# Kernel optimization log

Measured on AMD Instinct MI355X. Metric: run time of the kernel, lower is better.

## Reference

```python
import jax, jax.numpy as jnp
import numpy as np

E = 768
H = 8
EXP = 4
HEAD_D = E // H  # 96, also the post-softmax scaling factor


def _layernorm(x, g, b, eps=1e-5):
    mu = jnp.mean(x, axis=-1, keepdims=True)
    var = jnp.var(x, axis=-1, keepdims=True)
    return (x - mu) * jax.lax.rsqrt(var + eps) * g + b


def setup_inputs() -> dict:
    key = jax.random.key(0)
    ks = jax.random.split(key, 12)
    s = 0.02
    inp = {
        "x": jax.random.normal(ks[0], (8, 1024, E), dtype=jnp.float32),
        "ln1_g": jnp.ones((E,), jnp.float32),
        "ln1_b": jnp.zeros((E,), jnp.float32),
        "Wq": jax.random.normal(ks[1], (E, E), jnp.float32) * s,
        "bq": jnp.zeros((E,), jnp.float32),
        "Wk": jax.random.normal(ks[2], (E, E), jnp.float32) * s,
        "bk": jnp.zeros((E,), jnp.float32),
        "Wv": jax.random.normal(ks[3], (E, E), jnp.float32) * s,
        "bv": jnp.zeros((E,), jnp.float32),
        "Wo": jax.random.normal(ks[4], (E, E), jnp.float32) * s,
        "bo": jnp.zeros((E,), jnp.float32),
        "ln2_g": jnp.ones((E,), jnp.float32),
        "ln2_b": jnp.zeros((E,), jnp.float32),
        "W1": jax.random.normal(ks[5], (E, EXP * E), jnp.float32) * s,
        "b1": jnp.zeros((EXP * E,), jnp.float32),
        "W2": jax.random.normal(ks[6], (EXP * E, E), jnp.float32) * s,
        "b2": jnp.zeros((E,), jnp.float32),
    }
    return inp


def reference(x, ln1_g, ln1_b, Wq, bq, Wk, bk, Wv, bv, Wo, bo,
              ln2_g, ln2_b, W1, b1, W2, b2):
    B, N, _ = x.shape
    # --- sub_block_1: LN -> MHA (post-softmax scaling) -> residual ---
    h = _layernorm(x, ln1_g, ln1_b)
    q = (h @ Wq + bq).reshape(B, N, H, HEAD_D).transpose(0, 2, 1, 3)
    k = (h @ Wk + bk).reshape(B, N, H, HEAD_D).transpose(0, 2, 1, 3)
    v = (h @ Wv + bv).reshape(B, N, H, HEAD_D).transpose(0, 2, 1, 3)
    energy = jnp.einsum('bhqd,bhkd->bhqk', q, k)  # NOTE: no pre-softmax scale
    att = jax.nn.softmax(energy, axis=-1) * HEAD_D  # quirky post-softmax scaling
    out = jnp.einsum('bhqk,bhkd->bhqd', att, v)
    out = out.transpose(0, 2, 1, 3).reshape(B, N, E)
    out = out @ Wo + bo
    x = x + out  # residual
    # --- sub_block_2: LN -> GELU-FFN (NO residual, faithful to source) ---
    h = _layernorm(x, ln2_g, ln2_b)
    h = jax.nn.gelu(h @ W1 + b1, approximate=False)
    return h @ W2 + b2
```

## Files before the change

### kernel.cpp

```cpp
#include <hip/hip_runtime.h>
#include <hip/hip_bf16.h>
#include <math.h>

#define DI __device__ __forceinline__

typedef __attribute__((ext_vector_type(8))) __bf16 bf16x8;
typedef __attribute__((ext_vector_type(8))) short short8;
typedef __attribute__((ext_vector_type(4))) float f32x4;
typedef __attribute__((ext_vector_type(4))) int int4v;
typedef __attribute__((ext_vector_type(4))) unsigned short ushort4v;

DI short f2bfn(float f) {
  __bf16 b = (__bf16)f;
  short s;
  __builtin_memcpy(&s, &b, 2);
  return s;
}

DI float erf_fast(float x) {
  const float ax = fabsf(x);
  const float t = __builtin_amdgcn_rcpf(1.0f + 0.3275911f * ax);
  float p = 1.061405429f;
  p = p * t - 1.453152027f;
  p = p * t + 1.421413741f;
  p = p * t - 0.284496736f;
  p = p * t + 0.254829592f;
  p = p * t;
  const float r = 1.0f - p * __expf(-ax * ax);
  return copysignf(r, x);
}

DI void gload_lds16(const void* g, void* l) {
  __builtin_amdgcn_global_load_lds(
      (const __attribute__((address_space(1))) void*)g,
      (__attribute__((address_space(3))) void*)l, 16, 0, 0);
}

__global__ __launch_bounds__(256) void weight_prep(
    const float* __restrict__ Wq, const float* __restrict__ Wk,
    const float* __restrict__ Wv, const float* __restrict__ Wo,
    const float* __restrict__ W1, const float* __restrict__ W2,
    const float* __restrict__ bq, const float* __restrict__ bk,
    const float* __restrict__ bv,
    short* __restrict__ Wtqkv, short* __restrict__ Wto,
    short* __restrict__ Wt1, short* __restrict__ Wt2,
    float* __restrict__ bqkv)
{
  const int id = blockIdx.x, t = threadIdx.x;
  if (id >= 6912) {
    const int j = id - 6912;
    const float* src = j == 0 ? bq : (j == 1 ? bk : bv);
    for (int e = t; e < 768; e += 256) bqkv[j * 768 + e] = src[e];
    return;
  }
  const float* in;
  short* out;
  int K, N, bx, by;
  if (id < 2304) {
    const int w = id / 576, r2 = id % 576;
    bx = r2 % 24; by = r2 / 24; K = 768; N = 768;
    in = (w == 0) ? Wq : (w == 1) ? Wk : (w == 2) ? Wv : Wo;
    out = (w < 3) ? Wtqkv + (size_t)w * 768 * 768 : Wto;
  } else if (id < 4608) {
    const int r2 = id - 2304;
    bx = r2 % 96; by = r2 / 96; K = 768; N = 3072; in = W1; out = Wt1;
  } else {
    const int r2 = id - 4608;
    bx = r2 % 24; by = r2 / 24; K = 3072; N = 768; in = W2; out = Wt2;
  }
  __shared__ float tile[32][33];
  const int tx = t & 31, ty = t >> 5;
  const int n0 = bx * 32, k0 = by * 32;
#pragma unroll
  for (int p = 0; p < 4; ++p)
    tile[ty + p * 8][tx] = in[(size_t)(k0 + ty + p * 8) * N + n0 + tx];
  __syncthreads();
#pragma unroll
  for (int p = 0; p < 4; ++p)
    out[(size_t)(n0 + ty + p * 8) * K + k0 + tx] = f2bfn(tile[tx][ty + p * 8]);
}

__global__ __launch_bounds__(256) void ln_rows(
    const float* __restrict__ x, const float* __restrict__ gw,
    const float* __restrict__ bw, unsigned short* __restrict__ out)
{
  const int wv = threadIdx.x >> 6, ln = threadIdx.x & 63;
  const size_t row = (size_t)blockIdx.x * 4 + wv;
  const float* xr = x + row * 768;
  float4 v[3];
  float s = 0.f, sq = 0.f;
#pragma unroll
  for (int i = 0; i < 3; ++i) {
    v[i] = *(const float4*)(xr + i * 256 + ln * 4);
    s  += v[i].x + v[i].y + v[i].z + v[i].w;
    sq += v[i].x * v[i].x + v[i].y * v[i].y + v[i].z * v[i].z + v[i].w * v[i].w;
  }
#pragma unroll
  for (int msk = 1; msk < 64; msk <<= 1) {
    s  += __shfl_xor(s, msk);
    sq += __shfl_xor(sq, msk);
  }
  const float mean = s * (1.f / 768.f);
  const float var  = sq * (1.f / 768.f) - mean * mean;
  const float rstd = rsqrtf(var + 1e-5f);
#pragma unroll
  for (int i = 0; i < 3; ++i) {
    const int c = i * 256 + ln * 4;
    const float vals[4] = {v[i].x, v[i].y, v[i].z, v[i].w};
    ushort4v o;
#pragma unroll
    for (int j = 0; j < 4; ++j)
      o[j] = (unsigned short)f2bfn((vals[j] - mean) * rstd * gw[c + j] + bw[c + j]);
    *(ushort4v*)(out + row * 768 + c) = o;
  }
}

enum { EPI_BF16 = 0, EPI_F32_RES = 1, EPI_BF16_GELU = 2, EPI_F32 = 3, EPI_QKV = 4 };

template <int MODE, int BM, int BK, int MW>
__global__ __launch_bounds__(256, MW) void gemm_bt(
    const short* __restrict__ A,
    const short* __restrict__ Bt,
    const float* __restrict__ bias,
    const float* __restrict__ resid,
    void* __restrict__ Cout, short* __restrict__ vTout,
    int ldc, int Ntiles, int K)
{
  constexpr int NCHUNK = BK / 8;
  constexpr int CMASK = NCHUNK - 1;
  constexpr int ABYTES = BM * BK * 2;
  constexpr int STAGE_BYTES = (BM + 128) * BK * 2;
  constexpr int NLA = BM * BK / 8 / 256;
  constexpr int NLB = 128 * BK / 8 / 256;
  constexpr int LOADS = NLA + NLB;
  constexpr int MR = BM / 32;
  constexpr int NKK = BK / 32;
  constexpr int SMEM = 2 * STAGE_BYTES > 4 * 4352 ? 2 * STAGE_BYTES : 4 * 4352;
  __shared__ __align__(16) char smem[SMEM];
  const int t = threadIdx.x;
  const int wv = t >> 6, ln = t & 63;
  const int g = ln >> 4, r = ln & 15;
  const int sw = ((int)blockIdx.x & 7) * ((int)gridDim.x >> 3) + ((int)blockIdx.x >> 3);
  const int bm = sw / Ntiles, bn = sw % Ntiles;
  const int wr = wv >> 1, wc = wv & 1;
  f32x4 acc[MR][4] = {};

  const char* aptr[NLA];
  const char* bptr[NLB];
#pragma unroll
  for (int q = 0; q < NLA; ++q) {
    const int p = q * 256 + t;
    const int row = p / NCHUNK, c = (p & CMASK) ^ (row & CMASK);
    aptr[q] = (const char*)(A + (size_t)(bm * BM + row) * K + c * 8);
  }
#pragma unroll
  for (int q = 0; q < NLB; ++q) {
    const int p = q * 256 + t;
    const int row = p / NCHUNK, c = (p & CMASK) ^ (row & CMASK);
    bptr[q] = (const char*)(Bt + (size_t)(bn * 128 + row) * K + c * 8);
  }

  auto stage = [&](int buf) {
    char* as = smem + buf * STAGE_BYTES;
    char* bs = as + ABYTES;
#pragma unroll
    for (int q = 0; q < NLA; ++q) {
      gload_lds16(aptr[q], as + q * 4096 + wv * 1024);
      aptr[q] += BK * 2;
    }
#pragma unroll
    for (int q = 0; q < NLB; ++q) {
      gload_lds16(bptr[q], bs + q * 4096 + wv * 1024);
      bptr[q] += BK * 2;
    }
  };

  const int nk = K / BK;
  stage(0);
  stage(1);
  int cur = 0;
  for (int kt = 0; kt < nk; ++kt) {
    if (kt + 1 < nk)
      asm volatile("s_waitcnt vmcnt(%0)\n\ts_barrier" :: "n"(LOADS) : "memory");
    else
      asm volatile("s_waitcnt vmcnt(0)\n\ts_barrier" ::: "memory");
    const short* as = (const short*)(smem + cur * STAGE_BYTES);
    const short* bs = as + ABYTES / 2;
    bf16x8 af[MR][NKK], bfr[4][NKK];
#pragma unroll
    for (int m = 0; m < MR; ++m) {
      const int row = wr * (BM / 2) + m * 16 + r;
#pragma unroll
      for (int kk = 0; kk < NKK; ++kk)
        af[m][kk] = *(const bf16x8*)(as + row * BK + (((kk * 4 + g) ^ (row & CMASK)) << 3));
    }
#pragma unroll
    for (int n = 0; n < 4; ++n) {
      const int row = wc * 64 + n * 16 + r;
#pragma unroll
      for (int kk = 0; kk < NKK; ++kk)
        bfr[n][kk] = *(const bf16x8*)(bs + row * BK + (((kk * 4 + g) ^ (row & CMASK)) << 3));
    }
#pragma unroll
    for (int kk = 0; kk < NKK; ++kk)
#pragma unroll
      for (int m = 0; m < MR; ++m)
#pragma unroll
        for (int n = 0; n < 4; ++n)
          acc[m][n] = __builtin_amdgcn_mfma_f32_16x16x32_bf16(af[m][kk], bfr[n][kk],
                                                              acc[m][n], 0, 0, 0);
    if (kt + 2 < nk) {
      asm volatile("s_waitcnt lgkmcnt(0)\n\ts_barrier" ::: "memory");
      stage(cur);
    }
    cur ^= 1;
  }
  __syncthreads();

  float* epi = (float*)(smem + wv * 4352);

  if constexpr (MODE == EPI_QKV) {
    if (bn * 128 >= 1536) {
      const int tc = ln;
      const int cglob = bn * 128 + wc * 64 + tc;
      const int cv = cglob - 1536;
      const float bvs = bias[cglob];
#pragma unroll
      for (int m = 0; m < MR; ++m) {
#pragma unroll
        for (int n = 0; n < 4; ++n)
#pragma unroll
          for (int q = 0; q < 4; ++q)
            epi[(g * 4 + q) * 68 + n * 16 + r] = acc[m][n][q];
        float tv[16];
#pragma unroll
        for (int row = 0; row < 16; ++row) tv[row] = epi[row * 68 + tc] + bvs;
        const int tokbase = bm * BM + wr * (BM / 2) + m * 16;
        const int bb = tokbase >> 10, toff = tokbase & 1023;
        short8 o0, o1;
#pragma unroll
        for (int e = 0; e < 8; ++e) { o0[e] = f2bfn(tv[e]); o1[e] = f2bfn(tv[e + 8]); }
        short* dst = vTout + ((size_t)(bb * 768 + cv)) * 1024 + toff;
        *(short8*)dst = o0;
        *(short8*)(dst + 8) = o1;
      }
      return;
    }
  }

  const int cq = (ln & 3) * 16;
  const int lr = ln >> 2;
  const int c0 = bn * 128 + wc * 64 + cq;
  f32x4 bv[4];
#pragma unroll
  for (int j = 0; j < 4; ++j) bv[j] = *(const f32x4*)(bias + c0 + j * 4);

#pragma unroll
  for (int m = 0; m < MR; ++m) {
#pragma unroll
    for (int n = 0; n < 4; ++n)
#pragma unroll
      for (int q = 0; q < 4; ++q)
        epi[(g * 4 + q) * 68 + n * 16 + r] = acc[m][n][q];
    const size_t grow = (size_t)(bm * BM + wr * (BM / 2) + m * 16 + lr);
    float vals[16];
#pragma unroll
    for (int j = 0; j < 4; ++j) {
      const f32x4 vv = *(const f32x4*)(epi + lr * 68 + cq + j * 4);
#pragma unroll
      for (int e = 0; e < 4; ++e) vals[j * 4 + e] = vv[e] + bv[j][e];
    }
    if constexpr (MODE == EPI_F32_RES) {
#pragma unroll
      for (int j = 0; j < 4; ++j) {
        const f32x4 rv = *(const f32x4*)(resid + grow * ldc + c0 + j * 4);
#pragma unroll
        for (int e = 0; e < 4; ++e) vals[j * 4 + e] += rv[e];
      }
    }
    if constexpr (MODE == EPI_BF16_GELU) {
#pragma unroll
      for (int j = 0; j < 16; ++j)
        vals[j] = 0.5f * vals[j] * (1.0f + erf_fast(vals[j] * 0.70710678118654752f));
    }
    if constexpr (MODE == EPI_F32 || MODE == EPI_F32_RES) {
      float* op = (float*)Cout + grow * ldc + c0;
#pragma unroll
      for (int j = 0; j < 4; ++j) {
        f32x4 ov;
#pragma unroll
        for (int e = 0; e < 4; ++e) ov[e] = vals[j * 4 + e];
        *(f32x4*)(op + j * 4) = ov;
      }
    } else {
      unsigned short* op = (unsigned short*)Cout + grow * ldc + c0;
#pragma unroll
      for (int hhalf = 0; hhalf < 2; ++hhalf) {
        short8 ov;
#pragma unroll
        for (int e = 0; e < 8; ++e) ov[e] = f2bfn(vals[hhalf * 8 + e]);
        *(short8*)(op + hhalf * 8) = ov;
      }
    }
  }
}

__global__ __launch_bounds__(256, 2) void attn_fwd(
    const short* __restrict__ qkv, const short* __restrict__ vT,
    unsigned short* __restrict__ ab)
{
  __shared__ short Ks[2][64 * 128];
  __shared__ short Vs[2][96 * 64];
  __shared__ short Ps[4][2][16 * 64];
  const int t = threadIdx.x, wv = t >> 6, ln = t & 63;
  const int g = ln >> 4, r = ln & 15;
  const int bid = ((int)blockIdx.x & 7) * 64 + ((int)blockIdx.x >> 3);
  const int bh = bid >> 3, qt = bid & 7;
  const int b = bh >> 3, h = bh & 7;

  bf16x8 qf[2][3];
#pragma unroll
  for (int u = 0; u < 2; ++u) {
    const size_t rowq = (size_t)(b * 1024 + qt * 128 + wv * 32 + u * 16 + r);
#pragma unroll
    for (int kd = 0; kd < 3; ++kd)
      qf[u][kd] = *(const bf16x8*)(qkv + rowq * 2304 + h * 96 + kd * 32 + g * 8);
  }

  size_t offK[4];
#pragma unroll
  for (int i = 0; i < 4; ++i) {
    const int p = i * 256 + t;
    const int row = p >> 4, cb = p & 15, cbs = cb ^ (row & 7);
    offK[i] = (size_t)row * 2304 + 768 + h * 96 + (cbs << 3);
  }
  size_t offV[3];
#pragma unroll
  for (int i = 0; i < 3; ++i) {
    const int p = i * 256 + t;
    const int row = p >> 3, cb = p & 7, cbs = cb ^ (row & 7);
    offV[i] = ((size_t)bh * 96 + row) * 1024 + (cbs << 3);
  }
  const short* qb = qkv + (size_t)b * 1024 * 2304;

  auto stageKV = [&](int buf, int kt) {
    const size_t kadd = (size_t)kt * 64 * 2304;
#pragma unroll
    for (int i = 0; i < 4; ++i)
      gload_lds16(qb + kadd + offK[i], (char*)Ks[buf] + i * 4096 + wv * 1024);
#pragma unroll
    for (int i = 0; i < 3; ++i)
      gload_lds16(vT + offV[i] + kt * 64, (char*)Vs[buf] + i * 4096 + wv * 1024);
  };

  f32x4 o[2][6] = {};
  float mr[2] = {-1e30f, -1e30f}, lr[2] = {0.f, 0.f};

  stageKV(0, 0);
  __syncthreads();
  int cur = 0;
  for (int kt = 0; kt < 16; ++kt) {
    if (kt < 15) stageKV(cur ^ 1, kt + 1);
    const short* ks = Ks[cur];
    const short* vs = Vs[cur];

    f32x4 s[2][4] = {};
    __builtin_amdgcn_s_setprio(1);
#pragma unroll
    for (int sub = 0; sub < 4; ++sub) {
      bf16x8 kf[3];
#pragma unroll
      for (int kd = 0; kd < 3; ++kd)
        kf[kd] = *(const bf16x8*)(
            ks + (sub * 16 + r) * 128 + (((kd * 4 + g) ^ (r & 7)) << 3));
#pragma unroll
      for (int u = 0; u < 2; ++u)
#pragma unroll
        for (int kd = 0; kd < 3; ++kd)
          s[u][sub] = __builtin_amdgcn_mfma_f32_16x16x32_bf16(kf[kd], qf[u][kd],
                                                              s[u][sub], 0, 0, 0);
    }
    __builtin_amdgcn_s_setprio(0);

#pragma unroll
    for (int u = 0; u < 2; ++u) {
      float tm = fmaxf(fmaxf(s[u][0][0], s[u][0][1]),
                       fmaxf(s[u][0][2], s[u][0][3]));
#pragma unroll
      for (int sub = 1; sub < 4; ++sub)
        tm = fmaxf(tm, fmaxf(fmaxf(s[u][sub][0], s[u][sub][1]),
                             fmaxf(s[u][sub][2], s[u][sub][3])));
      tm = fmaxf(tm, __shfl_xor(tm, 16));
      tm = fmaxf(tm, __shfl_xor(tm, 32));

      if (__any(tm > mr[u] + 8.f)) {
        const float mnew = fmaxf(mr[u], tm);
        const float sc = __expf(mr[u] - mnew);
        lr[u] *= sc;
        mr[u] = mnew;
        float scr[4];
#pragma unroll
        for (int reg = 0; reg < 4; ++reg)
          scr[reg] = __shfl(sc, (ln & 48) | (g * 4 + reg));
#pragma unroll
        for (int nd = 0; nd < 6; ++nd)
#pragma unroll
          for (int reg = 0; reg < 4; ++reg) o[u][nd][reg] *= scr[reg];
      }

      float tsum = 0.f;
#pragma unroll
      for (int sub = 0; sub < 4; ++sub) {
        float p0 = __expf(s[u][sub][0] - mr[u]);
        float p1 = __expf(s[u][sub][1] - mr[u]);
        float p2 = __expf(s[u][sub][2] - mr[u]);
        float p3 = __expf(s[u][sub][3] - mr[u]);
        tsum += (p0 + p1) + (p2 + p3);
        ushort4v pk;
        pk[0] = (unsigned short)f2bfn(p0);
        pk[1] = (unsigned short)f2bfn(p1);
        pk[2] = (unsigned short)f2bfn(p2);
        pk[3] = (unsigned short)f2bfn(p3);
        const int c8 = (sub * 4 + g) ^ ((r & 7) << 1);
        *(ushort4v*)((char*)Ps[wv][u] + r * 128 + c8 * 8) = pk;
      }
      tsum += __shfl_xor(tsum, 16);
      tsum += __shfl_xor(tsum, 32);
      lr[u] += tsum;
    }

    bf16x8 pf[2][2];
#pragma unroll
    for (int u = 0; u < 2; ++u)
#pragma unroll
      for (int kk = 0; kk < 2; ++kk)
        pf[u][kk] = *(const bf16x8*)(
            Ps[wv][u] + r * 64 + (((kk * 4 + g) ^ (r & 7)) << 3));
    __builtin_amdgcn_s_setprio(1);
#pragma unroll
    for (int nd = 0; nd < 6; ++nd) {
      bf16x8 vf[2];
#pragma unroll
      for (int kk = 0; kk < 2; ++kk)
        vf[kk] = *(const bf16x8*)(
            vs + (nd * 16 + r) * 64 + (((kk * 4 + g) ^ (r & 7)) << 3));
#pragma unroll
      for (int u = 0; u < 2; ++u)
#pragma unroll
        for (int kk = 0; kk < 2; ++kk)
          o[u][nd] = __builtin_amdgcn_mfma_f32_16x16x32_bf16(pf[u][kk], vf[kk],
                                                             o[u][nd], 0, 0, 0);
    }
    __builtin_amdgcn_s_setprio(0);

    __syncthreads();
    cur ^= 1;
  }

#pragma unroll
  for (int u = 0; u < 2; ++u) {
    float linv[4];
#pragma unroll
    for (int reg = 0; reg < 4; ++reg)
      linv[reg] = 96.0f / __shfl(lr[u], (ln & 48) | (g * 4 + reg));
#pragma unroll
    for (int reg = 0; reg < 4; ++reg) {
      const size_t row = (size_t)(b * 1024 + qt * 128 + wv * 32 + u * 16 + g * 4 + reg);
#pragma unroll
      for (int nd = 0; nd < 6; ++nd)
        ab[row * 768 + h * 96 + nd * 16 + r] =
            (unsigned short)f2bfn(o[u][nd][reg] * linv[reg]);
    }
  }
}

extern "C" void kernel_launch(void* const* d_in, const int* in_sizes, int n_in,
                              void* d_out, int out_size, void* d_ws, size_t ws_size,
                              hipStream_t stream)
{
  const float* x    = (const float*)d_in[0];
  const float* ln1g = (const float*)d_in[1];
  const float* ln1b = (const float*)d_in[2];
  const float* Wq   = (const float*)d_in[3];
  const float* bq   = (const float*)d_in[4];
  const float* Wk   = (const float*)d_in[5];
  const float* bk   = (const float*)d_in[6];
  const float* Wv   = (const float*)d_in[7];
  const float* bv   = (const float*)d_in[8];
  const float* Wo   = (const float*)d_in[9];
  const float* bo   = (const float*)d_in[10];
  const float* ln2g = (const float*)d_in[11];
  const float* ln2b = (const float*)d_in[12];
  const float* W1   = (const float*)d_in[13];
  const float* b1   = (const float*)d_in[14];
  const float* W2   = (const float*)d_in[15];
  const float* b2   = (const float*)d_in[16];

  char* ws = (char*)d_ws;
  size_t off = 0;
  short* Wtqkv = (short*)(ws + off); off += (size_t)2304 * 768 * 2;
  short* Wto   = (short*)(ws + off); off += (size_t)768 * 768 * 2;
  short* Wt1   = (short*)(ws + off); off += (size_t)3072 * 768 * 2;
  short* Wt2   = (short*)(ws + off); off += (size_t)768 * 3072 * 2;
  float* bqkv  = (float*)(ws + off); off += 16384;
  short* hb    = (short*)(ws + off); off += (size_t)8192 * 768 * 2;
  short* qkv   = (short*)(ws + off); off += (size_t)8192 * 2304 * 2;
  short* h2b   = (short*)(ws + off); off += (size_t)8192 * 768 * 2;
  short* f1 = hb;
  short* ab = hb;
  short* vT = h2b;
  float* x1 = (float*)d_out;

  weight_prep<<<6915, 256, 0, stream>>>(Wq, Wk, Wv, Wo, W1, W2, bq, bk, bv,
                                        Wtqkv, Wto, Wt1, Wt2, bqkv);

  ln_rows<<<2048, 256, 0, stream>>>(x, ln1g, ln1b, (unsigned short*)hb);
  gemm_bt<EPI_QKV, 128, 32, 4><<<64 * 18, 256, 0, stream>>>(
      hb, Wtqkv, bqkv, nullptr, qkv, vT, 2304, 18, 768);
  attn_fwd<<<512, 256, 0, stream>>>(qkv, vT, (unsigned short*)ab);
  gemm_bt<EPI_F32_RES, 64, 64, 3><<<128 * 6, 256, 0, stream>>>(
      ab, Wto, bo, x, x1, nullptr, 768, 6, 768);

  ln_rows<<<2048, 256, 0, stream>>>(x1, ln2g, ln2b, (unsigned short*)h2b);
  gemm_bt<EPI_BF16_GELU, 128, 32, 4><<<64 * 24, 256, 0, stream>>>(
      h2b, Wt1, b1, nullptr, f1, nullptr, 3072, 24, 768);
  gemm_bt<EPI_F32, 64, 64, 3><<<128 * 6, 256, 0, stream>>>(
      f1, Wt2, b2, nullptr, (float*)d_out, nullptr, 768, 6, 3072);
}
```

Measured before the change: 242.3 us.

## Triple-buffer LDS stages in BM=128 GEMMs to drop per-iteration barrier

Adds an NBUF template parameter to the GEMM kernel. The QKV and FFN1 GEMMs (BM=128, BK=32) now use three LDS stage buffers. With a third buffer, the next global-to-LDS prefetch can be issued before the MFMA loop, and the second lgkmcnt wait plus barrier per k-iteration can be dropped, so loads overlap compute better. In exchange LDS use per block grows to three stages, and the occupancy hint drops from 4 to 3 blocks per CU for those GEMMs.

```diff
diff --git a/kernel.cpp b/kernel.cpp
--- a/kernel.cpp
+++ b/kernel.cpp
@@ -117,7 +117,7 @@
 
 enum { EPI_BF16 = 0, EPI_F32_RES = 1, EPI_BF16_GELU = 2, EPI_F32 = 3, EPI_QKV = 4 };
 
-template <int MODE, int BM, int BK, int MW>
+template <int MODE, int BM, int BK, int MW, int NBUF>
 __global__ __launch_bounds__(256, MW) void gemm_bt(
     const short* __restrict__ A,
     const short* __restrict__ Bt,
@@ -135,7 +135,8 @@
   constexpr int LOADS = NLA + NLB;
   constexpr int MR = BM / 32;
   constexpr int NKK = BK / 32;
-  constexpr int SMEM = 2 * STAGE_BYTES > 4 * 4352 ? 2 * STAGE_BYTES : 4 * 4352;
+  constexpr int SMEM = NBUF * STAGE_BYTES > 4 * 4352 ? NBUF * STAGE_BYTES
+                                                     : 4 * 4352;
   __shared__ __align__(16) char smem[SMEM];
   const int t = threadIdx.x;
   const int wv = t >> 6, ln = t & 63;
@@ -178,13 +179,13 @@
   const int nk = K / BK;
   stage(0);
   stage(1);
-  int cur = 0;
+  int rb = 0;
   for (int kt = 0; kt < nk; ++kt) {
     if (kt + 1 < nk)
       asm volatile("s_waitcnt vmcnt(%0)\n\ts_barrier" :: "n"(LOADS) : "memory");
     else
       asm volatile("s_waitcnt vmcnt(0)\n\ts_barrier" ::: "memory");
-    const short* as = (const short*)(smem + cur * STAGE_BYTES);
+    const short* as = (const short*)(smem + rb * STAGE_BYTES);
     const short* bs = as + ABYTES / 2;
     bf16x8 af[MR][NKK], bfr[4][NKK];
 #pragma unroll
@@ -201,19 +202,35 @@
       for (int kk = 0; kk < NKK; ++kk)
         bfr[n][kk] = *(const bf16x8*)(bs + row * BK + (((kk * 4 + g) ^ (row & CMASK)) << 3));
     }
-#pragma unroll
-    for (int kk = 0; kk < NKK; ++kk)
-#pragma unroll
-      for (int m = 0; m < MR; ++m)
-#pragma unroll
-        for (int n = 0; n < 4; ++n)
-          acc[m][n] = __builtin_amdgcn_mfma_f32_16x16x32_bf16(af[m][kk], bfr[n][kk],
-                                                              acc[m][n], 0, 0, 0);
-    if (kt + 2 < nk) {
-      asm volatile("s_waitcnt lgkmcnt(0)\n\ts_barrier" ::: "memory");
-      stage(cur);
-    }
-    cur ^= 1;
+    if constexpr (NBUF == 3) {
+      if (kt + 2 < nk) {
+        int sb = rb + 2; if (sb >= 3) sb -= 3;
+        stage(sb);
+      }
+#pragma unroll
+      for (int kk = 0; kk < NKK; ++kk)
+#pragma unroll
+        for (int m = 0; m < MR; ++m)
+#pragma unroll
+          for (int n = 0; n < 4; ++n)
+            acc[m][n] = __builtin_amdgcn_mfma_f32_16x16x32_bf16(af[m][kk], bfr[n][kk],
+                                                                acc[m][n], 0, 0, 0);
+      rb = rb == 2 ? 0 : rb + 1;
+    } else {
+#pragma unroll
+      for (int kk = 0; kk < NKK; ++kk)
+#pragma unroll
+        for (int m = 0; m < MR; ++m)
+#pragma unroll
+          for (int n = 0; n < 4; ++n)
+            acc[m][n] = __builtin_amdgcn_mfma_f32_16x16x32_bf16(af[m][kk], bfr[n][kk],
+                                                                acc[m][n], 0, 0, 0);
+      if (kt + 2 < nk) {
+        asm volatile("s_waitcnt lgkmcnt(0)\n\ts_barrier" ::: "memory");
+        stage(rb);
+      }
+      rb ^= 1;
+    }
   }
   __syncthreads();
 
@@ -515,15 +532,15 @@
                                         Wtqkv, Wto, Wt1, Wt2, bqkv);
 
   ln_rows<<<2048, 256, 0, stream>>>(x, ln1g, ln1b, (unsigned short*)hb);
-  gemm_bt<EPI_QKV, 128, 32, 4><<<64 * 18, 256, 0, stream>>>(
+  gemm_bt<EPI_QKV, 128, 32, 3, 3><<<64 * 18, 256, 0, stream>>>(
       hb, Wtqkv, bqkv, nullptr, qkv, vT, 2304, 18, 768);
   attn_fwd<<<512, 256, 0, stream>>>(qkv, vT, (unsigned short*)ab);
-  gemm_bt<EPI_F32_RES, 64, 64, 3><<<128 * 6, 256, 0, stream>>>(
+  gemm_bt<EPI_F32_RES, 64, 64, 3, 2><<<128 * 6, 256, 0, stream>>>(
       ab, Wto, bo, x, x1, nullptr, 768, 6, 768);
 
   ln_rows<<<2048, 256, 0, stream>>>(x1, ln2g, ln2b, (unsigned short*)h2b);
-  gemm_bt<EPI_BF16_GELU, 128, 32, 4><<<64 * 24, 256, 0, stream>>>(
+  gemm_bt<EPI_BF16_GELU, 128, 32, 3, 3><<<64 * 24, 256, 0, stream>>>(
       h2b, Wt1, b1, nullptr, f1, nullptr, 3072, 24, 768);
-  gemm_bt<EPI_F32, 64, 64, 3><<<128 * 6, 256, 0, stream>>>(
+  gemm_bt<EPI_F32, 64, 64, 3, 2><<<128 * 6, 256, 0, stream>>>(
       f1, Wt2, b2, nullptr, (float*)d_out, nullptr, 768, 6, 3072);
 }
```

Result: no change. 240.7 us (-0.7%).
